# Performance work log

Hardware: AMD Instinct MI355X
Metric: run time of the kernel (lower is better)

Reference implementation:

```python
import jax, jax.numpy as jnp
import numpy as np

B, T, K = 8192, 512, 12
START_TAG, STOP_TAG = 10, 11  # '[CLS]', '[SEP]' indices in default tag_map


def setup_inputs() -> dict:
    key = jax.random.key(0)
    k1, k2 = jax.random.split(key)
    logits = jax.random.normal(k1, (B, T, K), dtype=jnp.float32)
    transitions = jax.random.normal(k2, (K, K), dtype=jnp.float32)
    # constraints applied in BiLSTMCRF.__init__
    transitions = transitions.at[:, START_TAG].set(-1000.0)
    transitions = transitions.at[STOP_TAG, :].set(-1000.0)
    return {"logits": logits, "transitions": transitions}


def reference(logits, transitions):
    """Batched Viterbi decode, matching BiLSTMCRF.__viterbi_decode.

    logits: [B, T, K] emission scores (output of hidden2tag)
    transitions: [K, K] transitions[i, j] = score of tag i -> tag j
    Returns (scores [B], paths [B, T] int32).
    """
    em = jnp.swapaxes(logits, 0, 1)  # [T, B, K]

    def step(prev, emit_t):
        # prev: [B, K] trellis at t-1; v[b, i, j] = prev[b, i] + trans[i, j]
        v = prev[:, :, None] + transitions[None, :, :]  # [B, K, K]
        best = jnp.max(v, axis=1) + emit_t              # [B, K]
        bp = jnp.argmax(v, axis=1).astype(jnp.int32)    # [B, K]
        return best, bp

    final, bps = jax.lax.scan(step, em[0], em[1:])  # final: [B,K], bps: [T-1,B,K]

    scores = jnp.max(final, axis=-1)                     # [B]
    last = jnp.argmax(final, axis=-1).astype(jnp.int32)  # [B], tag at t = T-1

    def back(nxt, bp_t):
        # bp_t[b, j] = best previous tag given tag j at the next step
        cur = jnp.take_along_axis(bp_t, nxt[:, None], axis=1)[:, 0]
        return cur, cur

    # reverse scan: processes bps[T-2] .. bps[0], outputs tags for t = 0 .. T-2
    _, rest = jax.lax.scan(back, last, bps, reverse=True)  # [T-1, B]
    paths = jnp.concatenate([rest, last[None, :]], axis=0)  # [T, B]
    return scores, jnp.swapaxes(paths, 0, 1)
```

## Files before the change

kernel.cpp:

```cpp
#include <hip/hip_runtime.h>
#include <stdint.h>


namespace {

constexpr int kB = 8192;
constexpr int kT = 512;
constexpr int kK = 12;
constexpr int kW = 128;

template <int CTRL>
__device__ __forceinline__ float dppb(float x) {
    return __int_as_float(__builtin_amdgcn_update_dpp(
        0, __float_as_int(x), CTRL, 0xf, 0xf, true));
}

__global__ __launch_bounds__(256, 2) void viterbi_fused(
    const float* __restrict__ logits,
    const float* __restrict__ trans,
    float* __restrict__ out,
    uint32_t* __restrict__ bpw)
{
    __shared__ __align__(64) float xch[16][16];

    const int tid = blockIdx.x * 256 + threadIdx.x;
    const int b   = tid >> 4;
    const int j   = threadIdx.x & 15;
    const int g   = threadIdx.x >> 4;
    const int jeff = (j < kK) ? j : (kK - 1);
    const int chunk = ((j & 3) == 3) ? 2 : (j & 3);

    float* __restrict__ xg = &xch[g][0];
    const float4* __restrict__ xgc = (const float4*)(xg + 4 * chunk);

    const float T0  = trans[0*kK+jeff],  T1  = trans[1*kK+jeff];
    const float T2  = trans[2*kK+jeff],  T3  = trans[3*kK+jeff];
    const float T4  = trans[4*kK+jeff],  T5  = trans[5*kK+jeff];
    const float T6  = trans[6*kK+jeff],  T7  = trans[7*kK+jeff];
    const float T8  = trans[8*kK+jeff],  T9  = trans[9*kK+jeff];
    const float T10 = trans[10*kK+jeff], T11 = trans[11*kK+jeff];

    const float* __restrict__ em = logits + (size_t)b * kT * kK + jeff;
    uint32_t* __restrict__ bpb = bpw + (size_t)b * kW * kK;

    float prev = em[0];

    float e0 = em[1*kK], e1 = em[2*kK], e2 = em[3*kK], e3 = em[4*kK];
    float e4 = em[5*kK], e5 = em[6*kK], e6 = em[7*kK], e7 = em[8*kK];

    uint32_t packed = 0;

#define EMLOAD(t) em[((t) < kT ? (t) : (kT - 1)) * kK]

#define EXCHANGE()                                                           \
    xg[j] = prev;                                                            \
    const float4 Q = *xgc;                                                   \
    const float p0 = dppb<0x00>(Q.x), p1 = dppb<0x00>(Q.y);                  \
    const float p2 = dppb<0x00>(Q.z), p3 = dppb<0x00>(Q.w);                  \
    const float p4 = dppb<0x55>(Q.x), p5 = dppb<0x55>(Q.y);                  \
    const float p6 = dppb<0x55>(Q.z), p7 = dppb<0x55>(Q.w);                  \
    const float p8 = dppb<0xAA>(Q.x), p9 = dppb<0xAA>(Q.y);                  \
    const float p10 = dppb<0xAA>(Q.z), p11 = dppb<0xAA>(Q.w)

#define STEP(K, WBASE, EMIT) do {                                            \
    EXCHANGE();                                                              \
    const float c0 = p0 + T0,   c1 = p1 + T1;                                \
    const float c2 = p2 + T2,   c3 = p3 + T3;                                \
    const float c4 = p4 + T4,   c5 = p5 + T5;                                \
    const float c6 = p6 + T6,   c7 = p7 + T7;                                \
    const float c8 = p8 + T8,   c9 = p9 + T9;                                \
    const float c10 = p10 + T10, c11 = p11 + T11;                            \
    const float m0 = fmaxf(fmaxf(c0, c1), c2);                               \
    const float m1 = fmaxf(fmaxf(c3, c4), c5);                               \
    const float m2 = fmaxf(fmaxf(c6, c7), c8);                               \
    const float m3 = fmaxf(fmaxf(c9, c10), c11);                             \
    const float best = fmaxf(fmaxf(m0, m1), fmaxf(m2, m3));                  \
    int bi = 11;                                                             \
    bi = (c10 == best) ? 10 : bi;  bi = (c9 == best) ? 9 : bi;               \
    bi = (c8  == best) ?  8 : bi;  bi = (c7 == best) ? 7 : bi;               \
    bi = (c6  == best) ?  6 : bi;  bi = (c5 == best) ? 5 : bi;               \
    bi = (c4  == best) ?  4 : bi;  bi = (c3 == best) ? 3 : bi;               \
    bi = (c2  == best) ?  2 : bi;  bi = (c1 == best) ? 1 : bi;               \
    bi = (c0  == best) ?  0 : bi;                                            \
    prev = best + (EMIT);                                                    \
    packed |= (uint32_t)bi << (8 * ((K) & 3));                               \
    if (((K) & 3) == 3) {                                                    \
        if (j < kK) bpb[(size_t)((WBASE) + ((K) >> 2)) * kK + j] = packed;   \
        packed = 0;                                                          \
    }                                                                        \
} while (0)

    for (int n = 0; n < 63; ++n) {
        const int tb = 8 * n + 1;
        const int w0 = 2 * n;
        const float f0 = EMLOAD(tb + 8),  f1 = EMLOAD(tb + 9);
        const float f2 = EMLOAD(tb + 10), f3 = EMLOAD(tb + 11);
        const float f4 = EMLOAD(tb + 12), f5 = EMLOAD(tb + 13);
        const float f6 = EMLOAD(tb + 14), f7 = EMLOAD(tb + 15);

        STEP(0, w0, e0); STEP(1, w0, e1); STEP(2, w0, e2); STEP(3, w0, e3);
        STEP(4, w0, e4); STEP(5, w0, e5); STEP(6, w0, e6); STEP(7, w0, e7);

        e0 = f0; e1 = f1; e2 = f2; e3 = f3;
        e4 = f4; e5 = f5; e6 = f6; e7 = f7;
    }

    STEP(0, 126, e0); STEP(1, 126, e1); STEP(2, 126, e2); STEP(3, 126, e3);
    STEP(4, 126, e4); STEP(5, 126, e5); STEP(6, 126, e6);
    if (j < kK) bpb[(size_t)127 * kK + j] = packed;

#undef STEP
#undef EMLOAD

    float best, v0, v1, v2, v3, v4, v5, v6, v7, v8, v9, v10, v11;
    {
        EXCHANGE();
        v0 = p0; v1 = p1; v2 = p2; v3 = p3; v4 = p4; v5 = p5;
        v6 = p6; v7 = p7; v8 = p8; v9 = p9; v10 = p10; v11 = p11;
        const float n0 = fmaxf(fmaxf(v0, v1), v2);
        const float n1 = fmaxf(fmaxf(v3, v4), v5);
        const float n2 = fmaxf(fmaxf(v6, v7), v8);
        const float n3 = fmaxf(fmaxf(v9, v10), v11);
        best = fmaxf(fmaxf(n0, n1), fmaxf(n2, n3));
    }
    int last = 11;
    last = (v10 == best) ? 10 : last;  last = (v9 == best) ? 9 : last;
    last = (v8  == best) ?  8 : last;  last = (v7 == best) ? 7 : last;
    last = (v6  == best) ?  6 : last;  last = (v5 == best) ? 5 : last;
    last = (v4  == best) ?  4 : last;  last = (v3 == best) ? 3 : last;
    last = (v2  == best) ?  2 : last;  last = (v1 == best) ? 1 : last;
    last = (v0  == best) ?  0 : last;

#undef EXCHANGE

    __syncthreads();

    if (j == 0) {
        out[b] = best;
        float* __restrict__ paths = out + kB + (size_t)b * kT;
        paths[kT - 1] = (float)last;

        int tag = last;
        const uint4* __restrict__ r = (const uint4*)bpb;
#pragma unroll 4
        for (int w = kW - 1; w >= 0; --w) {
            const uint4 q0 = r[w * 3 + 0];
            const uint4 q1 = r[w * 3 + 1];
            const uint4 q2 = r[w * 3 + 2];
            const int smax = (w == kW - 1) ? 510 : (w * 4 + 3);
            for (int s = smax; s >= w * 4; --s) {
                const uint32_t ax = (tag & 8) ? q2.x : ((tag & 4) ? q1.x : q0.x);
                const uint32_t ay = (tag & 8) ? q2.y : ((tag & 4) ? q1.y : q0.y);
                const uint32_t az = (tag & 8) ? q2.z : ((tag & 4) ? q1.z : q0.z);
                const uint32_t aw = (tag & 8) ? q2.w : ((tag & 4) ? q1.w : q0.w);
                const uint32_t lo = (tag & 1) ? ay : ax;
                const uint32_t hi = (tag & 1) ? aw : az;
                const uint32_t dw = (tag & 2) ? hi : lo;
                tag = (int)((dw >> (8 * (s & 3))) & 0xFF);
                paths[s] = (float)tag;
            }
        }
    }
}

}

extern "C" void kernel_launch(void* const* d_in, const int* in_sizes, int n_in,
                              void* d_out, int out_size, void* d_ws, size_t ws_size,
                              hipStream_t stream) {
    const float* logits = (const float*)d_in[0];
    const float* trans  = (const float*)d_in[1];
    float* out = (float*)d_out;
    uint32_t* bpw = (uint32_t*)d_ws;

    const int threads = 256;
    const int blocks = (kB * 16) / threads;
    viterbi_fused<<<blocks, threads, 0, stream>>>(logits, trans, out, bpw);
}
```

Measured before the change: 510.7 us.

## Stream emissions into LDS via async global_load_lds double buffering

```diff
diff --git a/kernel.cpp b/kernel.cpp
--- a/kernel.cpp
+++ b/kernel.cpp
@@ -8,6 +8,7 @@
 constexpr int kT = 512;
 constexpr int kK = 12;
 constexpr int kW = 128;
+constexpr int kRowF = 392;
 
 template <int CTRL>
 __device__ __forceinline__ float dppb(float x) {
@@ -22,16 +23,19 @@
     uint32_t* __restrict__ bpw)
 {
     __shared__ __align__(64) float xch[16][16];
-
-    const int tid = blockIdx.x * 256 + threadIdx.x;
-    const int b   = tid >> 4;
-    const int j   = threadIdx.x & 15;
-    const int g   = threadIdx.x >> 4;
+    __shared__ __align__(16) float embuf[2][16][kRowF];
+
+    const int j    = threadIdx.x & 15;
+    const int g    = threadIdx.x >> 4;
+    const int wv   = threadIdx.x >> 6;
+    const int ln   = threadIdx.x & 63;
+    const int brow0 = blockIdx.x * 16;
+    const int b    = brow0 + g;
     const int jeff = (j < kK) ? j : (kK - 1);
-    const int chunk = ((j & 3) == 3) ? 2 : (j & 3);
+    const int xsel = ((j & 3) == 3) ? 2 : (j & 3);
 
     float* __restrict__ xg = &xch[g][0];
-    const float4* __restrict__ xgc = (const float4*)(xg + 4 * chunk);
+    const float4* __restrict__ xgc = (const float4*)(xg + 4 * xsel);
 
     const float T0  = trans[0*kK+jeff],  T1  = trans[1*kK+jeff];
     const float T2  = trans[2*kK+jeff],  T3  = trans[3*kK+jeff];
@@ -40,17 +44,43 @@
     const float T8  = trans[8*kK+jeff],  T9  = trans[9*kK+jeff];
     const float T10 = trans[10*kK+jeff], T11 = trans[11*kK+jeff];
 
-    const float* __restrict__ em = logits + (size_t)b * kT * kK + jeff;
     uint32_t* __restrict__ bpb = bpw + (size_t)b * kW * kK;
 
-    float prev = em[0];
-
-    float e0 = em[1*kK], e1 = em[2*kK], e2 = em[3*kK], e3 = em[4*kK];
-    float e4 = em[5*kK], e5 = em[6*kK], e6 = em[7*kK], e7 = em[8*kK];
+#define DMA_CHUNK(c) do {                                                     \
+    const int dsel_ = (c) & 1;                                                \
+    const float* sbase_ = logits + (size_t)(brow0 + 4 * wv) * 6144            \
+                          + (c) * 384 + ln;                                   \
+    _Pragma("unroll")                                                         \
+    for (int r4_ = 0; r4_ < 4; ++r4_) {                                       \
+        _Pragma("unroll")                                                     \
+        for (int p_ = 0; p_ < 6; ++p_) {                                      \
+            const float* gsrc_ = sbase_ + r4_ * 6144 + p_ * 64;               \
+            float* ldst_ = &embuf[dsel_][4 * wv + r4_][p_ * 64];              \
+            __builtin_amdgcn_global_load_lds(                                 \
+                (const __attribute__((address_space(1))) void*)gsrc_,         \
+                (__attribute__((address_space(3))) void*)ldst_, 4, 0, 0);     \
+        }                                                                     \
+    }                                                                         \
+} while (0)
+
+    auto emrd = [&](int t) -> float {
+        const int tc = (t < kT) ? t : (kT - 1);
+        return embuf[(tc >> 5) & 1][g][(tc & 31) * 12 + jeff];
+    };
+
+    DMA_CHUNK(0);
+    DMA_CHUNK(1);
+
+    float prev = logits[(size_t)b * 6144 + jeff];
+
+    __builtin_amdgcn_wave_barrier();
+    __builtin_amdgcn_s_waitcnt(0x0F70);
+    __builtin_amdgcn_wave_barrier();
+
+    float e0 = emrd(1), e1 = emrd(2), e2 = emrd(3), e3 = emrd(4);
+    float e4 = emrd(5), e5 = emrd(6), e6 = emrd(7), e7 = emrd(8);
 
     uint32_t packed = 0;
-
-#define EMLOAD(t) em[((t) < kT ? (t) : (kT - 1)) * kK]
 
 #define EXCHANGE()                                                           \
     xg[j] = prev;                                                            \
@@ -93,10 +123,26 @@
     for (int n = 0; n < 63; ++n) {
         const int tb = 8 * n + 1;
         const int w0 = 2 * n;
-        const float f0 = EMLOAD(tb + 8),  f1 = EMLOAD(tb + 9);
-        const float f2 = EMLOAD(tb + 10), f3 = EMLOAD(tb + 11);
-        const float f4 = EMLOAD(tb + 12), f5 = EMLOAD(tb + 13);
-        const float f6 = EMLOAD(tb + 14), f7 = EMLOAD(tb + 15);
+
+        if ((n & 3) == 2) {
+            __builtin_amdgcn_wave_barrier();
+            __builtin_amdgcn_s_waitcnt(0x0F70);
+            __builtin_amdgcn_wave_barrier();
+        }
+        if ((n & 3) == 3) {
+            const int cc = (n >> 2) + 2;
+            if (cc <= 15) {
+                __builtin_amdgcn_wave_barrier();
+                __builtin_amdgcn_s_waitcnt(0xC07F);
+                DMA_CHUNK(cc);
+                __builtin_amdgcn_wave_barrier();
+            }
+        }
+
+        const float f0 = emrd(tb + 8),  f1 = emrd(tb + 9);
+        const float f2 = emrd(tb + 10), f3 = emrd(tb + 11);
+        const float f4 = emrd(tb + 12), f5 = emrd(tb + 13);
+        const float f6 = emrd(tb + 14), f7 = emrd(tb + 15);
 
         STEP(0, w0, e0); STEP(1, w0, e1); STEP(2, w0, e2); STEP(3, w0, e3);
         STEP(4, w0, e4); STEP(5, w0, e5); STEP(6, w0, e6); STEP(7, w0, e7);
@@ -110,7 +156,7 @@
     if (j < kK) bpb[(size_t)127 * kK + j] = packed;
 
 #undef STEP
-#undef EMLOAD
+#undef DMA_CHUNK
 
     float best, v0, v1, v2, v3, v4, v5, v6, v7, v8, v9, v10, v11;
     {
@@ -174,6 +220,6 @@
     uint32_t* bpw = (uint32_t*)d_ws;
 
     const int threads = 256;
-    const int blocks = (kB * 16) / threads;
+    const int blocks = kB / 16;
     viterbi_fused<<<blocks, threads, 0, stream>>>(logits, trans, out, bpw);
 }
```

Result: no change. 510.4 us (-0.1%).
